# Kernel optimization log

Measured on AMD Instinct MI355X. Metric: run time of the kernel, lower is better.

## Reference

```python
import jax, jax.numpy as jnp
import numpy as np

EMBED_DIM = 1024
NUM_HEADS = 16
HEAD_DIM = EMBED_DIM // NUM_HEADS


def setup_inputs() -> dict:
    key = jax.random.key(0)
    ks = jax.random.split(key, 5)
    s = 1.0 / np.sqrt(EMBED_DIM)
    x = jax.random.normal(ks[0], (2, 2048, EMBED_DIM), dtype=jnp.float32)
    Wq = jax.random.normal(ks[1], (EMBED_DIM, EMBED_DIM), dtype=jnp.float32) * s
    Wk = jax.random.normal(ks[2], (EMBED_DIM, EMBED_DIM), dtype=jnp.float32) * s
    Wv = jax.random.normal(ks[3], (EMBED_DIM, EMBED_DIM), dtype=jnp.float32) * s
    Wo = jax.random.normal(ks[4], (EMBED_DIM, EMBED_DIM), dtype=jnp.float32) * s
    z = jnp.zeros((EMBED_DIM,), dtype=jnp.float32)
    return {"x": x, "Wq": Wq, "bq": z, "Wk": Wk, "bk": z, "Wv": Wv, "bv": z, "Wo": Wo, "bo": z}


def reference(x, Wq, bq, Wk, bk, Wv, bv, Wo, bo):
    B, S, E = x.shape
    H, D = NUM_HEADS, HEAD_DIM
    # projections; weights stored as [in, out] so y = x @ W + b
    q = (x @ Wq + bq).reshape(B, S, H, D).transpose(0, 2, 1, 3)  # [B,H,S,D]
    k = (x @ Wk + bk).reshape(B, S, H, D).transpose(0, 2, 1, 3)
    v = (x @ Wv + bv).reshape(B, S, H, D).transpose(0, 2, 1, 3)
    scores = jnp.einsum('bhqd,bhkd->bhqk', q, k) / jnp.sqrt(jnp.float32(D))
    attn = jax.nn.softmax(scores, axis=-1)
    out = jnp.einsum('bhqk,bhkd->bhqd', attn, v)  # [B,H,S,D]
    out = out.transpose(0, 2, 1, 3).reshape(B, S, E)
    return out @ Wo + bo
```

## Files before the change

### kernel.cpp

```cpp
#include <hip/hip_runtime.h>
#include <cstdint>
#include <cstddef>

typedef __attribute__((ext_vector_type(8))) short bf16x8;
typedef __attribute__((ext_vector_type(4))) float f32x4;
typedef __attribute__((ext_vector_type(16))) float f32x16;
typedef __attribute__((ext_vector_type(4))) unsigned int u32x4;
typedef __attribute__((ext_vector_type(2))) unsigned int u32x2;

__device__ __forceinline__ unsigned short f2bf(float f) {
    union { float f; unsigned int u; } c; c.f = f;
    unsigned int r = c.u + 0x7FFFu + ((c.u >> 16) & 1u);
    return (unsigned short)(r >> 16);
}
__device__ __forceinline__ unsigned int pack2bf(float a, float b) {
    return (unsigned int)f2bf(a) | ((unsigned int)f2bf(b) << 16);
}
__device__ __forceinline__ unsigned int cvtpk(float lo, float hi) {
    unsigned int r;
    asm("v_cvt_pk_bf16_f32 %0, %1, %2" : "=v"(r) : "v"(lo), "v"(hi));
    return r;
}
__device__ __forceinline__ void gload16(const void* g, void* l) {
    __builtin_amdgcn_global_load_lds((const __attribute__((address_space(1))) void*)g,
                                     (__attribute__((address_space(3))) void*)l, 16, 0, 0);
}

__global__ __launch_bounds__(256) void cvt_x_kernel(const float* __restrict__ src,
                                                    unsigned short* __restrict__ dst) {
    int e = (blockIdx.x * 256 + threadIdx.x) * 8;
    const float4* s4 = reinterpret_cast<const float4*>(src + e);
    float4 a = s4[0], b = s4[1];
    u32x4 o;
    o.x = pack2bf(a.x, a.y); o.y = pack2bf(a.z, a.w);
    o.z = pack2bf(b.x, b.y); o.w = pack2bf(b.z, b.w);
    *reinterpret_cast<u32x4*>(dst + e) = o;
}

__global__ __launch_bounds__(256) void cvt_w_kernel(const float* __restrict__ w0,
    const float* __restrict__ w1, const float* __restrict__ w2, const float* __restrict__ w3,
    unsigned short* __restrict__ dstbase) {
    __shared__ unsigned short sm[64][68];
    int z = blockIdx.y;
    const float* src = (z == 0) ? w0 : (z == 1) ? w1 : (z == 2) ? w2 : w3;
    unsigned short* dst = dstbase + (size_t)z * 1048576;
    int n0 = (blockIdx.x & 15) * 64;
    int k0 = (blockIdx.x >> 4) * 64;
    int tid = threadIdx.x;
    #pragma unroll
    for (int i = 0; i < 4; i++) {
        int e = i * 1024 + tid * 4;
        int r = e >> 6, c = e & 63;
        float4 v = *reinterpret_cast<const float4*>(src + (size_t)(k0 + r) * 1024 + n0 + c);
        u32x2 p; p.x = pack2bf(v.x, v.y); p.y = pack2bf(v.z, v.w);
        *reinterpret_cast<u32x2*>(&sm[r][c]) = p;
    }
    __syncthreads();
    #pragma unroll
    for (int i = 0; i < 4; i++) {
        int e = i * 1024 + tid * 4;
        int n = e >> 6, kk = e & 63;
        u32x2 p;
        p.x = (unsigned)sm[kk][n]     | ((unsigned)sm[kk + 1][n] << 16);
        p.y = (unsigned)sm[kk + 2][n] | ((unsigned)sm[kk + 3][n] << 16);
        *reinterpret_cast<u32x2*>(dst + (size_t)(n0 + n) * 1024 + k0 + kk) = p;
    }
}

__device__ __forceinline__ void gemm128_main(
    const unsigned short* __restrict__ A, const unsigned short* __restrict__ Wt,
    int m0, int n0, int tid,
    unsigned short* Asm, unsigned short* Bsm,
    f32x4 acc[4][4])
{
    const int lane = tid & 63;
    const int w = tid >> 6;
    const int wm = w >> 1, wn = w & 1;
    const int lr = lane & 15, lg = lane >> 4;
    for (int k0 = 0; k0 < 1024; k0 += 64) {
        __syncthreads();
        #pragma unroll
        for (int i = 0; i < 4; i++) {
            int L = (i * 4 + w) * 64 + lane;
            int r = L >> 3, cs = L & 7;
            int c = cs ^ (r & 7);
            gload16(A  + (size_t)(m0 + r) * 1024 + k0 + c * 8, Asm + (i * 4 + w) * 512);
            gload16(Wt + (size_t)(n0 + r) * 1024 + k0 + c * 8, Bsm + (i * 4 + w) * 512);
        }
        __syncthreads();
        #pragma unroll
        for (int ks = 0; ks < 2; ks++) {
            bf16x8 af[4], bfr[4];
            #pragma unroll
            for (int t = 0; t < 4; t++) {
                int Ra = wm * 64 + t * 16 + lr;
                af[t]  = *reinterpret_cast<const bf16x8*>(Asm + Ra * 64 + ((ks * 4 + lg) ^ (Ra & 7)) * 8);
                int Rb = wn * 64 + t * 16 + lr;
                bfr[t] = *reinterpret_cast<const bf16x8*>(Bsm + Rb * 64 + ((ks * 4 + lg) ^ (Rb & 7)) * 8);
            }
            #pragma unroll
            for (int mt = 0; mt < 4; mt++) {
                #pragma unroll
                for (int nt = 0; nt < 4; nt++)
                    acc[mt][nt] = __builtin_amdgcn_mfma_f32_16x16x32_bf16(af[mt], bfr[nt], acc[mt][nt], 0, 0, 0);
            }
        }
    }
}

__global__ __launch_bounds__(256) void gemm_qkv_kernel(
    const unsigned short* __restrict__ A, const unsigned short* __restrict__ WtBase,
    const float* __restrict__ bq, const float* __restrict__ bk, const float* __restrict__ bv,
    unsigned short* __restrict__ Qo, unsigned short* __restrict__ Ko, unsigned short* __restrict__ Vto)
{
    __shared__ unsigned short Asm[8192];
    __shared__ unsigned short Bsm[8192];
    const int z = blockIdx.z;
    const unsigned short* Wt = WtBase + (size_t)z * 1048576;
    const float* bias = (z == 0) ? bq : (z == 1) ? bk : bv;
    const int m0 = blockIdx.y * 128, n0 = blockIdx.x * 128;
    const int tid = threadIdx.x, lane = tid & 63, w = tid >> 6;
    const int wm = w >> 1, wn = w & 1, lr = lane & 15, lg = lane >> 4;
    f32x4 acc[4][4];
    f32x4 zero4 = {0.f, 0.f, 0.f, 0.f};
    #pragma unroll
    for (int i = 0; i < 4; i++)
        #pragma unroll
        for (int j = 0; j < 4; j++) acc[i][j] = zero4;
    gemm128_main(A, Wt, m0, n0, tid, Asm, Bsm, acc);

    const float qs = 0.125f * 1.44269504088896341f;
    #pragma unroll
    for (int mt = 0; mt < 4; mt++) {
        #pragma unroll
        for (int nt = 0; nt < 4; nt++) {
            int gn = n0 + wn * 64 + nt * 16 + lr;
            int h = gn >> 6, d = gn & 63;
            int rb = m0 + wm * 64 + mt * 16 + lg * 4;
            int b_ = rb >> 11, s = rb & 2047;
            float bv_ = bias[gn];
            if (z == 2) {
                u32x2 p;
                p.x = pack2bf(acc[mt][nt][0] + bv_, acc[mt][nt][1] + bv_);
                p.y = pack2bf(acc[mt][nt][2] + bv_, acc[mt][nt][3] + bv_);
                *reinterpret_cast<u32x2*>(Vto + ((size_t)(b_ * 16 + h) * 64 + d) * 2048 + s) = p;
            } else {
                unsigned short* dst = (z == 0) ? Qo : Ko;
                float sc_ = (z == 0) ? qs : 1.0f;
                #pragma unroll
                for (int r = 0; r < 4; r++)
                    dst[((size_t)(b_ * 16 + h) * 2048 + (s + r)) * 64 + d] = f2bf((acc[mt][nt][r] + bv_) * sc_);
            }
        }
    }
}

__global__ __launch_bounds__(256, 2) void attn_kernel(
    const unsigned short* __restrict__ Qg,
    const unsigned short* __restrict__ Kg,
    const unsigned short* __restrict__ Vtg,
    unsigned short* __restrict__ Og)
{
    __shared__ unsigned short Ksm[128][72];
    __shared__ unsigned short Vsm[64][136];

    const int tid = threadIdx.x, lane = tid & 63, w = tid >> 6;
    const int l31 = lane & 31, L = lane >> 5;
    const int bh = blockIdx.y, q0 = blockIdx.x * 128;
    const size_t kvbase = (size_t)bh * (2048 * 64);
    const size_t vtbase = (size_t)bh * (64 * 2048);

    {
        u32x4 qr[4];
        #pragma unroll
        for (int i = 0; i < 4; i++) {
            int ck = i * 256 + tid; int r = ck >> 3, c = (ck & 7) * 8;
            qr[i] = *reinterpret_cast<const u32x4*>(Qg + kvbase + (size_t)(q0 + r) * 64 + c);
        }
        #pragma unroll
        for (int i = 0; i < 4; i++) {
            int ck = i * 256 + tid; int r = ck >> 3, c = (ck & 7) * 8;
            *reinterpret_cast<u32x4*>(&Ksm[r][c]) = qr[i];
        }
    }
    __syncthreads();
    bf16x8 qf[4];
    #pragma unroll
    for (int ds = 0; ds < 4; ds++)
        qf[ds] = *reinterpret_cast<const bf16x8*>(&Ksm[w * 32 + l31][ds * 16 + L * 8]);
    __syncthreads();

    f32x16 oacc[2];
    #pragma unroll
    for (int dt = 0; dt < 2; dt++)
        #pragma unroll
        for (int j = 0; j < 16; j++) oacc[dt][j] = 0.f;
    float m_run = -3.0e38f, l_run = 0.f;

    u32x4 kreg[4], vreg[4];
#define LOAD_TILE(KV0)                                                                      \
    _Pragma("unroll")                                                                       \
    for (int i = 0; i < 4; i++) {                                                           \
        int ck = i * 256 + tid; int r = ck >> 3, c = (ck & 7) * 8;                          \
        kreg[i] = *reinterpret_cast<const u32x4*>(Kg + kvbase + (size_t)((KV0) + r) * 64 + c); \
        int dv = ck >> 4, cv = (ck & 15) * 8;                                               \
        vreg[i] = *reinterpret_cast<const u32x4*>(Vtg + vtbase + (size_t)dv * 2048 + (KV0) + cv); \
    }

    LOAD_TILE(0)
    for (int kt = 0; kt < 16; kt++) {
        #pragma unroll
        for (int i = 0; i < 4; i++) {
            int ck = i * 256 + tid; int r = ck >> 3, c = (ck & 7) * 8;
            *reinterpret_cast<u32x4*>(&Ksm[r][c]) = kreg[i];
            int dv = ck >> 4, cv = (ck & 15) * 8;
            *reinterpret_cast<u32x4*>(&Vsm[dv][cv]) = vreg[i];
        }
        __syncthreads();
        int kvn = (kt < 15) ? (kt + 1) * 128 : 0;
        LOAD_TILE(kvn)

        f32x16 sc[4];
        #pragma unroll
        for (int nt = 0; nt < 4; nt++) {
            #pragma unroll
            for (int j = 0; j < 16; j++) sc[nt][j] = 0.f;
            #pragma unroll
            for (int ds = 0; ds < 4; ds++) {
                bf16x8 kf = *reinterpret_cast<const bf16x8*>(&Ksm[nt * 32 + l31][ds * 16 + L * 8]);
                sc[nt] = __builtin_amdgcn_mfma_f32_32x32x16_bf16(kf, qf[ds], sc[nt], 0, 0, 0);
            }
        }

        float pmax = sc[0][0];
        #pragma unroll
        for (int nt = 0; nt < 4; nt++)
            #pragma unroll
            for (int j = 0; j < 16; j++) pmax = fmaxf(pmax, sc[nt][j]);
        pmax = fmaxf(pmax, __shfl_xor(pmax, 32));

        if (__any(pmax - m_run > 8.0f)) {
            float mnew = fmaxf(m_run, pmax);
            float f = __builtin_amdgcn_exp2f(m_run - mnew);
            l_run *= f;
            #pragma unroll
            for (int dt = 0; dt < 2; dt++)
                #pragma unroll
                for (int j = 0; j < 16; j++) oacc[dt][j] *= f;
            m_run = mnew;
        }

        float psum = 0.f;
        unsigned pdw[4][4][2];
        #pragma unroll
        for (int nt = 0; nt < 4; nt++) {
            float p[16];
            #pragma unroll
            for (int j = 0; j < 16; j++) {
                p[j] = __builtin_amdgcn_exp2f(sc[nt][j] - m_run);
                psum += p[j];
            }
            #pragma unroll
            for (int a = 0; a < 4; a++) {
                pdw[nt][a][0] = cvtpk(p[4 * a + 0], p[4 * a + 1]);
                pdw[nt][a][1] = cvtpk(p[4 * a + 2], p[4 * a + 3]);
            }
        }
        psum += __shfl_xor(psum, 32);
        l_run += psum;

        #pragma unroll
        for (int kt2 = 0; kt2 < 8; kt2++) {
            const int nt = kt2 >> 1, b2 = (kt2 & 1) * 2;
            unsigned own0  = L ? pdw[nt][b2 + 1][0] : pdw[nt][b2][0];
            unsigned own1  = L ? pdw[nt][b2 + 1][1] : pdw[nt][b2][1];
            unsigned send0 = L ? pdw[nt][b2][0]     : pdw[nt][b2 + 1][0];
            unsigned send1 = L ? pdw[nt][b2][1]     : pdw[nt][b2 + 1][1];
            unsigned recv0 = (unsigned)__shfl_xor((int)send0, 32);
            unsigned recv1 = (unsigned)__shfl_xor((int)send1, 32);
            u32x4 pf4;
            pf4.x = L ? recv0 : own0;
            pf4.y = L ? recv1 : own1;
            pf4.z = L ? own0  : recv0;
            pf4.w = L ? own1  : recv1;
            bf16x8 pfr = *reinterpret_cast<bf16x8*>(&pf4);
            #pragma unroll
            for (int dt = 0; dt < 2; dt++) {
                bf16x8 vf = *reinterpret_cast<const bf16x8*>(&Vsm[dt * 32 + l31][kt2 * 16 + L * 8]);
                oacc[dt] = __builtin_amdgcn_mfma_f32_32x32x16_bf16(vf, pfr, oacc[dt], 0, 0, 0);
            }
        }
        __syncthreads();
    }
#undef LOAD_TILE

    float inv = 1.0f / l_run;
    const int b_ = bh >> 4, h = bh & 15;
    const int s = q0 + w * 32 + l31;
    unsigned short* orow = Og + ((size_t)b_ * 2048 + s) * 1024 + h * 64;
    #pragma unroll
    for (int dt = 0; dt < 2; dt++) {
        #pragma unroll
        for (int g = 0; g < 4; g++) {
            u32x2 pp;
            pp.x = cvtpk(oacc[dt][4 * g + 0] * inv, oacc[dt][4 * g + 1] * inv);
            pp.y = cvtpk(oacc[dt][4 * g + 2] * inv, oacc[dt][4 * g + 3] * inv);
            *reinterpret_cast<u32x2*>(orow + dt * 32 + g * 8 + 4 * L) = pp;
        }
    }
}

__global__ __launch_bounds__(256) void gemm_out_kernel(
    const unsigned short* __restrict__ A, const unsigned short* __restrict__ Wt,
    const float* __restrict__ bias, float* __restrict__ out)
{
    __shared__ unsigned short Asm[8192];
    __shared__ unsigned short Bsm[8192];
    const int m0 = blockIdx.y * 128, n0 = blockIdx.x * 128;
    const int tid = threadIdx.x, lane = tid & 63, w = tid >> 6;
    const int wm = w >> 1, wn = w & 1, lr = lane & 15, lg = lane >> 4;
    f32x4 acc[4][4];
    f32x4 zero4 = {0.f, 0.f, 0.f, 0.f};
    #pragma unroll
    for (int i = 0; i < 4; i++)
        #pragma unroll
        for (int j = 0; j < 4; j++) acc[i][j] = zero4;
    gemm128_main(A, Wt, m0, n0, tid, Asm, Bsm, acc);
    #pragma unroll
    for (int mt = 0; mt < 4; mt++) {
        #pragma unroll
        for (int nt = 0; nt < 4; nt++) {
            int gn = n0 + wn * 64 + nt * 16 + lr;
            float bv_ = bias[gn];
            int rb = m0 + wm * 64 + mt * 16 + lg * 4;
            #pragma unroll
            for (int r = 0; r < 4; r++)
                out[(size_t)(rb + r) * 1024 + gn] = acc[mt][nt][r] + bv_;
        }
    }
}

extern "C" void kernel_launch(void* const* d_in, const int* in_sizes, int n_in,
                              void* d_out, int out_size, void* d_ws, size_t ws_size,
                              hipStream_t stream) {
    const float* x  = (const float*)d_in[0];
    const float* Wq = (const float*)d_in[1];
    const float* bq = (const float*)d_in[2];
    const float* Wk = (const float*)d_in[3];
    const float* bk = (const float*)d_in[4];
    const float* Wv = (const float*)d_in[5];
    const float* bv = (const float*)d_in[6];
    const float* Wo = (const float*)d_in[7];
    const float* bo = (const float*)d_in[8];
    float* out = (float*)d_out;

    if (ws_size < (size_t)25165824 * 2) return;
    unsigned short* ws  = (unsigned short*)d_ws;
    unsigned short* xbf = ws;
    unsigned short* wt  = ws + 4194304;
    unsigned short* Qb  = ws + 8388608;
    unsigned short* Kb  = ws + 12582912;
    unsigned short* Vtb = ws + 16777216;
    unsigned short* Ob  = ws + 20971520;

    cvt_x_kernel<<<2048, 256, 0, stream>>>(x, xbf);
    cvt_w_kernel<<<dim3(256, 4), 256, 0, stream>>>(Wq, Wk, Wv, Wo, wt);
    gemm_qkv_kernel<<<dim3(8, 32, 3), 256, 0, stream>>>(xbf, wt, bq, bk, bv, Qb, Kb, Vtb);
    attn_kernel<<<dim3(16, 32), 256, 0, stream>>>(Qb, Kb, Vtb, Ob);
    gemm_out_kernel<<<dim3(8, 32), 256, 0, stream>>>(Ob, wt + 3 * 1048576, bo, out);
}
```

Measured before the change: 136.4 us.

## Merge conversion kernels, remap GEMM blocks per XCD, tree-reduce softmax max/sum

Merges the x and weight bf16 conversion kernels into one launch, which removes a kernel launch and its gap. Both GEMMs switch to a 1-D grid whose block index is permuted so consecutive blocks land on the same XCD, aiming for better L2 reuse of A/B tiles. In the attention kernel the serial max and sum chains become tree reductions to shorten dependency latency. The P fragments are also built ahead of the PV MFMA loop so shuffles and MFMAs can overlap, at the cost of more live registers.

Measured after the change: 132.4 us. 1.03x faster.

```diff
diff --git a/kernel.cpp b/kernel.cpp
--- a/kernel.cpp
+++ b/kernel.cpp
@@ -25,28 +25,46 @@
     __builtin_amdgcn_global_load_lds((const __attribute__((address_space(1))) void*)g,
                                      (__attribute__((address_space(3))) void*)l, 16, 0, 0);
 }
-
-__global__ __launch_bounds__(256) void cvt_x_kernel(const float* __restrict__ src,
-                                                    unsigned short* __restrict__ dst) {
-    int e = (blockIdx.x * 256 + threadIdx.x) * 8;
-    const float4* s4 = reinterpret_cast<const float4*>(src + e);
-    float4 a = s4[0], b = s4[1];
-    u32x4 o;
-    o.x = pack2bf(a.x, a.y); o.y = pack2bf(a.z, a.w);
-    o.z = pack2bf(b.x, b.y); o.w = pack2bf(b.z, b.w);
-    *reinterpret_cast<u32x4*>(dst + e) = o;
-}
-
-__global__ __launch_bounds__(256) void cvt_w_kernel(const float* __restrict__ w0,
-    const float* __restrict__ w1, const float* __restrict__ w2, const float* __restrict__ w3,
-    unsigned short* __restrict__ dstbase) {
+__device__ __forceinline__ float tmax16(const f32x16& v) {
+    float a0 = fmaxf(v[0], v[1]),   a1 = fmaxf(v[2], v[3]);
+    float a2 = fmaxf(v[4], v[5]),   a3 = fmaxf(v[6], v[7]);
+    float a4 = fmaxf(v[8], v[9]),   a5 = fmaxf(v[10], v[11]);
+    float a6 = fmaxf(v[12], v[13]), a7 = fmaxf(v[14], v[15]);
+    float b0 = fmaxf(a0, a1), b1 = fmaxf(a2, a3);
+    float b2 = fmaxf(a4, a5), b3 = fmaxf(a6, a7);
+    return fmaxf(fmaxf(b0, b1), fmaxf(b2, b3));
+}
+__device__ __forceinline__ float tsum16(const float* p) {
+    float a0 = p[0] + p[1],   a1 = p[2] + p[3];
+    float a2 = p[4] + p[5],   a3 = p[6] + p[7];
+    float a4 = p[8] + p[9],   a5 = p[10] + p[11];
+    float a6 = p[12] + p[13], a7 = p[14] + p[15];
+    float b0 = a0 + a1, b1 = a2 + a3, b2 = a4 + a5, b3 = a6 + a7;
+    return (b0 + b1) + (b2 + b3);
+}
+
+__global__ __launch_bounds__(256) void cvt_kernel(const float* __restrict__ x,
+    const float* __restrict__ w0, const float* __restrict__ w1,
+    const float* __restrict__ w2, const float* __restrict__ w3,
+    unsigned short* __restrict__ xdst, unsigned short* __restrict__ wdst) {
     __shared__ unsigned short sm[64][68];
-    int z = blockIdx.y;
+    const int bid = blockIdx.x;
+    const int tid = threadIdx.x;
+    if (bid >= 1024) {
+        int e = ((bid - 1024) * 256 + tid) * 8;
+        const float4* s4 = reinterpret_cast<const float4*>(x + e);
+        float4 a = s4[0], b = s4[1];
+        u32x4 o;
+        o.x = pack2bf(a.x, a.y); o.y = pack2bf(a.z, a.w);
+        o.z = pack2bf(b.x, b.y); o.w = pack2bf(b.z, b.w);
+        *reinterpret_cast<u32x4*>(xdst + e) = o;
+        return;
+    }
+    int z = bid >> 8, xb = bid & 255;
     const float* src = (z == 0) ? w0 : (z == 1) ? w1 : (z == 2) ? w2 : w3;
-    unsigned short* dst = dstbase + (size_t)z * 1048576;
-    int n0 = (blockIdx.x & 15) * 64;
-    int k0 = (blockIdx.x >> 4) * 64;
-    int tid = threadIdx.x;
+    unsigned short* dst = wdst + (size_t)z * 1048576;
+    int n0 = (xb & 15) * 64;
+    int k0 = (xb >> 4) * 64;
     #pragma unroll
     for (int i = 0; i < 4; i++) {
         int e = i * 1024 + tid * 4;
@@ -115,10 +133,13 @@
 {
     __shared__ unsigned short Asm[8192];
     __shared__ unsigned short Bsm[8192];
-    const int z = blockIdx.z;
+    const int bid = blockIdx.x;
+    const int wg = (bid & 7) * 96 + (bid >> 3);
+    const int z = wg >> 8;
+    const int rem = wg & 255;
+    const int m0 = (rem >> 3) * 128, n0 = (rem & 7) * 128;
     const unsigned short* Wt = WtBase + (size_t)z * 1048576;
     const float* bias = (z == 0) ? bq : (z == 1) ? bk : bv;
-    const int m0 = blockIdx.y * 128, n0 = blockIdx.x * 128;
     const int tid = threadIdx.x, lane = tid & 63, w = tid >> 6;
     const int wm = w >> 1, wn = w & 1, lr = lane & 15, lg = lane >> 4;
     f32x4 acc[4][4];
@@ -232,11 +253,8 @@
             }
         }
 
-        float pmax = sc[0][0];
-        #pragma unroll
-        for (int nt = 0; nt < 4; nt++)
-            #pragma unroll
-            for (int j = 0; j < 16; j++) pmax = fmaxf(pmax, sc[nt][j]);
+        float pmax = fmaxf(fmaxf(tmax16(sc[0]), tmax16(sc[1])),
+                           fmaxf(tmax16(sc[2]), tmax16(sc[3])));
         pmax = fmaxf(pmax, __shfl_xor(pmax, 32));
 
         if (__any(pmax - m_run > 8.0f)) {
@@ -256,10 +274,9 @@
         for (int nt = 0; nt < 4; nt++) {
             float p[16];
             #pragma unroll
-            for (int j = 0; j < 16; j++) {
+            for (int j = 0; j < 16; j++)
                 p[j] = __builtin_amdgcn_exp2f(sc[nt][j] - m_run);
-                psum += p[j];
-            }
+            psum += tsum16(p);
             #pragma unroll
             for (int a = 0; a < 4; a++) {
                 pdw[nt][a][0] = cvtpk(p[4 * a + 0], p[4 * a + 1]);
@@ -269,6 +286,7 @@
         psum += __shfl_xor(psum, 32);
         l_run += psum;
 
+        bf16x8 pfr[8];
         #pragma unroll
         for (int kt2 = 0; kt2 < 8; kt2++) {
             const int nt = kt2 >> 1, b2 = (kt2 & 1) * 2;
@@ -283,11 +301,14 @@
             pf4.y = L ? recv1 : own1;
             pf4.z = L ? own0  : recv0;
             pf4.w = L ? own1  : recv1;
-            bf16x8 pfr = *reinterpret_cast<bf16x8*>(&pf4);
+            pfr[kt2] = *reinterpret_cast<bf16x8*>(&pf4);
+        }
+        #pragma unroll
+        for (int kt2 = 0; kt2 < 8; kt2++) {
             #pragma unroll
             for (int dt = 0; dt < 2; dt++) {
                 bf16x8 vf = *reinterpret_cast<const bf16x8*>(&Vsm[dt * 32 + l31][kt2 * 16 + L * 8]);
-                oacc[dt] = __builtin_amdgcn_mfma_f32_32x32x16_bf16(vf, pfr, oacc[dt], 0, 0, 0);
+                oacc[dt] = __builtin_amdgcn_mfma_f32_32x32x16_bf16(vf, pfr[kt2], oacc[dt], 0, 0, 0);
             }
         }
         __syncthreads();
@@ -316,7 +337,9 @@
 {
     __shared__ unsigned short Asm[8192];
     __shared__ unsigned short Bsm[8192];
-    const int m0 = blockIdx.y * 128, n0 = blockIdx.x * 128;
+    const int bid = blockIdx.x;
+    const int wg = (bid & 7) * 32 + (bid >> 3);
+    const int m0 = (wg >> 3) * 128, n0 = (wg & 7) * 128;
     const int tid = threadIdx.x, lane = tid & 63, w = tid >> 6;
     const int wm = w >> 1, wn = w & 1, lr = lane & 15, lg = lane >> 4;
     f32x4 acc[4][4];
@@ -363,9 +386,8 @@
     unsigned short* Vtb = ws + 16777216;
     unsigned short* Ob  = ws + 20971520;
 
-    cvt_x_kernel<<<2048, 256, 0, stream>>>(x, xbf);
-    cvt_w_kernel<<<dim3(256, 4), 256, 0, stream>>>(Wq, Wk, Wv, Wo, wt);
-    gemm_qkv_kernel<<<dim3(8, 32, 3), 256, 0, stream>>>(xbf, wt, bq, bk, bv, Qb, Kb, Vtb);
+    cvt_kernel<<<3072, 256, 0, stream>>>(x, Wq, Wk, Wv, Wo, xbf, wt);
+    gemm_qkv_kernel<<<768, 256, 0, stream>>>(xbf, wt, bq, bk, bv, Qb, Kb, Vtb);
     attn_kernel<<<dim3(16, 32), 256, 0, stream>>>(Qb, Kb, Vtb, Ob);
-    gemm_out_kernel<<<dim3(8, 32), 256, 0, stream>>>(Ob, wt + 3 * 1048576, bo, out);
-}
+    gemm_out_kernel<<<256, 256, 0, stream>>>(Ob, wt + 3 * 1048576, bo, out);
+}
```
